# Optimization experiments

Hardware: AMD Instinct MI355X
Metric: run time of the kernel (lower is better)

## Reference

```python
import jax, jax.numpy as jnp
import numpy as np

HEADS = 16
EPS = 1e-5

def _ln(t):
    # LayerNorm over last axis, no affine params
    mu = jnp.mean(t, axis=-1, keepdims=True)
    var = jnp.var(t, axis=-1, keepdims=True)
    return (t - mu) / jnp.sqrt(var + EPS)

def setup_inputs() -> dict:
    key = jax.random.key(0)
    ks = jax.random.split(key, 8)
    b, n, dim, mlp_dim = 4, 2048, 1024, 4096
    s = lambda d: 1.0 / np.sqrt(d)
    return {
        "x": jax.random.normal(ks[0], (b, n, dim), dtype=jnp.float32),
        "Wqkv": jax.random.uniform(ks[1], (dim, 3 * dim), jnp.float32, -s(dim), s(dim)),
        "W1": jax.random.uniform(ks[2], (dim, mlp_dim), jnp.float32, -s(dim), s(dim)),
        "b1": jax.random.uniform(ks[3], (mlp_dim,), jnp.float32, -s(dim), s(dim)),
        "W2": jax.random.uniform(ks[4], (mlp_dim, dim), jnp.float32, -s(mlp_dim), s(mlp_dim)),
        "b2": jax.random.uniform(ks[5], (dim,), jnp.float32, -s(mlp_dim), s(mlp_dim)),
        "Wout": jax.random.uniform(ks[6], (dim, dim), jnp.float32, -s(dim), s(dim)),
        "bout": jax.random.uniform(ks[7], (dim,), jnp.float32, -s(dim), s(dim)),
    }

def reference(x, Wqkv, W1, b1, W2, b2, Wout, bout):
    b, n, dim = x.shape
    h = HEADS
    d = dim // h
    scale = dim ** (-0.5)  # NOTE: module scales by full dim, not head_dim
    qkv = x @ Wqkv  # [b, n, 3*dim]
    qkv = qkv.reshape(b, n, 3, h, d).transpose(2, 0, 3, 1, 4)  # [3, b, h, n, d]
    q, k, v = qkv[0], qkv[1], qkv[2]
    q, k = _ln(q), _ln(k)
    dots = jnp.einsum('bhid,bhjd->bhij', q, k) * scale
    attn = jax.nn.softmax(dots, axis=-1)
    attn_v = jnp.einsum('bhij,bhjd->bhid', attn, v)
    attn_v = attn_v.transpose(0, 2, 1, 3).reshape(b, n, dim)
    attn_out = attn_v @ Wout + bout
    parallel = jax.nn.gelu(x @ W1 + b1, approximate=False) @ W2 + b2
    return _ln(attn_out + parallel)
```

## Files before the change

kernel.cpp:

```cpp
#include <hip/hip_runtime.h>

typedef __attribute__((ext_vector_type(8))) short s16x8;
typedef __attribute__((ext_vector_type(4))) short s16x4;
typedef __attribute__((ext_vector_type(4))) float f32x4;
typedef __attribute__((ext_vector_type(16))) float f32x16;
typedef __attribute__((ext_vector_type(2))) unsigned uint2v;

#define DEVINL __device__ __forceinline__

DEVINL float b2f(short u){ return __uint_as_float(((unsigned)(unsigned short)u) << 16); }
DEVINL short f2bf(float f){
  unsigned u = __float_as_uint(f);
  u += 0x7fffu + ((u >> 16) & 1u);
  return (short)(u >> 16);
}
DEVINL unsigned cvtpk(float lo, float hi){
  unsigned r;
  asm("v_cvt_pk_bf16_f32 %0, %1, %2" : "=v"(r) : "v"(lo), "v"(hi));
  return r;
}
DEVINL float max3f(float a, float b, float c){
  float r; asm("v_max3_f32 %0, %1, %2, %3" : "=v"(r) : "v"(a), "v"(b), "v"(c)); return r;
}

#if __has_builtin(__builtin_amdgcn_exp2f)
#define EXP2F __builtin_amdgcn_exp2f
#else
#define EXP2F exp2f
#endif

DEVINL f32x4 mfma32(s16x8 a, s16x8 b, f32x4 c){
  return __builtin_amdgcn_mfma_f32_16x16x32_bf16(a, b, c, 0, 0, 0);
}
DEVINL f32x16 mfma3216(s16x8 a, s16x8 b, f32x16 c){
  return __builtin_amdgcn_mfma_f32_32x32x16_bf16(a, b, c, 0, 0, 0);
}

DEVINL uint2v pl32swap(unsigned a, unsigned b){
#if __has_builtin(__builtin_amdgcn_permlane32_swap)
  return __builtin_amdgcn_permlane32_swap(a, b, false, false);
#else
  asm volatile("v_permlane32_swap_b32 %0, %1" : "+v"(a), "+v"(b));
  uint2v r; r[0] = a; r[1] = b; return r;
#endif
}

typedef const unsigned __attribute__((address_space(1)))* gas1;
typedef unsigned __attribute__((address_space(3)))* las3;
DEVINL void gload16(const short* g, short* l){
  __builtin_amdgcn_global_load_lds((gas1)g, (las3)l, 16, 0, 0);
}

#define CFENCE asm volatile("" ::: "memory")
#define PBAR  do{ CFENCE; __builtin_amdgcn_sched_barrier(0); __builtin_amdgcn_s_barrier(); \
                  __builtin_amdgcn_sched_barrier(0); CFENCE; }while(0)
#define VMW8 asm volatile("s_waitcnt vmcnt(8)" ::: "memory")
#define VMW4 asm volatile("s_waitcnt vmcnt(4)" ::: "memory")
#define VMW0 asm volatile("s_waitcnt vmcnt(0)" ::: "memory")
#define PRIO1 __builtin_amdgcn_s_setprio(1)
#define PRIO0 __builtin_amdgcn_s_setprio(0)

static const int Bc   = 4;
static const int Nc   = 2048;
static const int DIM  = 1024;
static const int Tc   = Bc * Nc;
static const int MLP  = 4096;
static const int D3   = 3072;

static const size_t OFF_XB    = 0;
static const size_t OFF_WQKVT = OFF_XB    + 16777216;
static const size_t OFF_W1T   = OFF_WQKVT + 6291456;
static const size_t OFF_W2T   = OFF_W1T   + 8388608;
static const size_t OFF_WOUTT = OFF_W2T   + 8388608;
static const size_t OFF_QKV   = OFF_WOUTT + 2097152;
static const size_t OFF_QLN   = OFF_QKV   + 50331648;
static const size_t OFF_KLN   = OFF_QLN   + 16777216;
static const size_t OFF_VT    = OFF_KLN   + 16777216;
static const size_t OFF_ATTNV = OFF_VT    + 16777216;
static const size_t OFF_H     = OFF_QKV;
static const size_t OFF_P2    = OFF_KLN;
static const size_t OFF_A2    = OFF_VT;

__global__ __launch_bounds__(256) void conv_x(const float* __restrict__ x, short* __restrict__ xb){
  size_t i = ((size_t)blockIdx.x * 256 + threadIdx.x) * 8;
  f32x4 v0 = *(const f32x4*)(x + i);
  f32x4 v1 = *(const f32x4*)(x + i + 4);
  s16x8 o;
#pragma unroll
  for (int j = 0; j < 4; ++j){ o[j] = f2bf(v0[j]); o[4+j] = f2bf(v1[j]); }
  *(s16x8*)(xb + i) = o;
}

__global__ __launch_bounds__(256) void transpose_conv(const float* __restrict__ W, short* __restrict__ Wt,
                                                      int K, int N){
  __shared__ float tile[32][33];
  int ntx = N >> 5;
  int tx = blockIdx.x % ntx, ty = blockIdx.x / ntx;
  int r = threadIdx.x >> 3, c = (threadIdx.x & 7) * 4;
  f32x4 v = *(const f32x4*)(W + (size_t)(ty*32 + r)*N + tx*32 + c);
  tile[r][c] = v[0]; tile[r][c+1] = v[1]; tile[r][c+2] = v[2]; tile[r][c+3] = v[3];
  __syncthreads();
  s16x4 o;
#pragma unroll
  for (int j = 0; j < 4; ++j) o[j] = f2bf(tile[c+j][r]);
  *(s16x4*)(Wt + (size_t)(tx*32 + r)*K + ty*32 + c) = o;
}

template<int ACT>
__global__ __launch_bounds__(256, 2) void gemmCF(const short* __restrict__ A, const short* __restrict__ Bt,
                                                 short* __restrict__ C, const float* __restrict__ bias,
                                                 int M, int N, int K){
  __shared__ short lds[32768];

  const int tid = threadIdx.x;
  const int w = tid >> 6, lane = tid & 63;
  const int lr = lane & 15, g = lane >> 4;
  const int wr = w >> 1, wc = w & 1;
  const int NT = K >> 6, NIT = NT >> 1;

  const int nbn = N >> 7;
  const int cpx = gridDim.x >> 3;
  const int bid = (int)blockIdx.x;
  const int sw = (bid & 7)*cpx + (bid >> 3);
  const int nbn8 = nbn >> 3;
  const int T8 = sw >> 6, t64 = sw & 63;
  const int bm = (T8 / nbn8)*8 + (t64 >> 3);
  const int bn = (T8 % nbn8)*8 + (t64 & 7);

  const int l2 = lane >> 2;
  const int gsw = ((lane & 3) - ((lane >> 3) & 3)) & 3;
  const int cof = gsw * 8;
  const int qsw8 = ((g + (lr >> 1)) & 3) * 8;

  const short* ap0 = A  + (size_t)(bm*128 + w*16 + l2)*K + cof;
  const short* bp0 = Bt + (size_t)(bn*128 + w*16 + l2)*K + cof;

#define STG(soff, src, T_, kk) do{ \
    gload16(src + (size_t)(T_)*64 + (kk)*32,                 lds + (soff) + w*512); \
    gload16(src + (size_t)64*K + (size_t)(T_)*64 + (kk)*32,  lds + (soff) + 2048 + w*512); }while(0)
#define STA(s, T_, kk) STG((s)*4096, ap0, T_, kk)
#define STB(s, T_, kk) STG(16384 + (s)*4096, bp0, T_, kk)
#define LDA(s, mi) (*(const s16x8*)&lds[(s)*4096 + (wr*64 + (mi)*16 + lr)*32 + qsw8])
#define LDB(s, ni) (*(const s16x8*)&lds[16384 + (s)*4096 + (wc*64 + (ni)*16 + lr)*32 + qsw8])

  f32x4 acc[4][4] = {};
#define MM(ai, r) \
  acc[r][0]=mfma32(ai,b0,acc[r][0]); acc[r][1]=mfma32(ai,b1,acc[r][1]); \
  acc[r][2]=mfma32(ai,b2,acc[r][2]); acc[r][3]=mfma32(ai,b3,acc[r][3]);
#define RD(s) s16x8 a0=LDA(s,0),a1=LDA(s,1),a2=LDA(s,2),a3=LDA(s,3), \
                    b0=LDB(s,0),b1=LDB(s,1),b2=LDB(s,2),b3=LDB(s,3);
#define MM16 MM(a0,0) MM(a1,1) MM(a2,2) MM(a3,3)

  STA(0,0,0); STB(0,0,0);
  STA(1,0,1); STB(1,0,1);
  STA(2,1,0); STB(2,1,0);
  VMW8;
  PBAR;

  for (int i = 0; i < NIT; ++i){
    const int t = i << 1;
    const bool more = (i + 1 < NIT);
    {
      RD(0)
      STA(3, t+1, 1); STB(3, t+1, 1);
      PBAR; PRIO1; MM16 PRIO0;
      VMW8;
      PBAR;
    }
    {
      RD(1)
      if (more){ STA(0, t+2, 0); STB(0, t+2, 0); }
      PBAR; PRIO1; MM16 PRIO0;
      if (more){ VMW8; } else { VMW4; }
      PBAR;
    }
    {
      RD(2)
      if (more){ STA(1, t+2, 1); STB(1, t+2, 1); }
      PBAR; PRIO1; MM16 PRIO0;
      if (more){ VMW8; } else { VMW0; }
      PBAR;
    }
    {
      RD(3)
      if (more){ STA(2, t+3, 0); STB(2, t+3, 0); }
      PBAR; PRIO1; MM16 PRIO0;
      if (more){ VMW8; }
      PBAR;
    }
  }
#undef MM
#undef RD
#undef MM16
#undef STG
#undef STA
#undef STB
#undef LDA
#undef LDB

#pragma unroll
  for (int a = 0; a < 4; ++a){
#pragma unroll
    for (int ni = 0; ni < 4; ++ni){
      const int col = wc*64 + ni*16 + lr;
      const float bv = bias ? bias[bn*128 + col] : 0.f;
      f32x4 v = acc[a][ni];
#pragma unroll
      for (int ii = 0; ii < 4; ++ii){
        float val = v[ii] + bv;
        if constexpr (ACT) val = 0.5f*val*(1.f + erff(val*0.70710678118f));
        lds[(wr*64 + a*16 + 4*g + ii)*128 + col] = f2bf(val);
      }
    }
  }
  __syncthreads();
  const size_t crow0 = (size_t)bm * 128;
  const int ch = (tid & 15) * 8;
#pragma unroll
  for (int p = 0; p < 8; ++p){
    const int row = p*16 + (tid >> 4);
    *(s16x8*)&C[(crow0 + row)*N + bn*128 + ch] = *(const s16x8*)&lds[row*128 + ch];
  }
}

__global__ __launch_bounds__(256) void ln_reorg(const short* __restrict__ qkv, short* __restrict__ qln,
                                                short* __restrict__ kln, short* __restrict__ vtb){
  __shared__ short vtile[64*72];
  int bh = blockIdx.x >> 5, tch = blockIdx.x & 31;
  int b = bh >> 4, h = bh & 15;
  int tq = threadIdx.x >> 2, j = threadIdx.x & 3;
  size_t row = (size_t)b*Nc + tch*64 + tq;
  const short* base = qkv + row*D3 + h*64 + j*16;
  size_t orow = ((size_t)bh*Nc + tch*64 + tq)*64 + j*16;

#pragma unroll
  for (int part = 0; part < 2; ++part){
    const short* src = base + part*DIM;
    s16x8 u0 = *(const s16x8*)src;
    s16x8 u1 = *(const s16x8*)(src + 8);
    float f[16]; float s = 0.f, sq = 0.f;
#pragma unroll
    for (int i = 0; i < 8; ++i){ f[i] = b2f(u0[i]); f[8+i] = b2f(u1[i]); }
#pragma unroll
    for (int i = 0; i < 16; ++i){ s += f[i]; sq += f[i]*f[i]; }
    s  += __shfl_xor(s, 1);  s  += __shfl_xor(s, 2);
    sq += __shfl_xor(sq, 1); sq += __shfl_xor(sq, 2);
    float mu = s * (1.f/64.f);
    float var = sq * (1.f/64.f) - mu*mu;
    float inv = rsqrtf(var + 1e-5f) * (part == 0 ? 0.04508422003f : 1.f);
    s16x8 o0, o1;
#pragma unroll
    for (int i = 0; i < 8; ++i){ o0[i] = f2bf((f[i]-mu)*inv); o1[i] = f2bf((f[8+i]-mu)*inv); }
    short* dst = (part == 0 ? qln : kln) + orow;
    *(s16x8*)dst = o0; *(s16x8*)(dst + 8) = o1;
  }

  s16x8 v0 = *(const s16x8*)(base + 2*DIM);
  s16x8 v1 = *(const s16x8*)(base + 2*DIM + 8);
  *(s16x8*)&vtile[tq*72 + j*16]     = v0;
  *(s16x8*)&vtile[tq*72 + j*16 + 8] = v1;
  __syncthreads();
  s16x8 o0, o1;
#pragma unroll
  for (int i = 0; i < 8; ++i){
    o0[i] = vtile[(j*16 + i)*72 + tq];
    o1[i] = vtile[(j*16 + 8 + i)*72 + tq];
  }
  short* vdst = vtb + ((size_t)bh*64 + tq)*Nc + tch*64 + j*16;
  *(s16x8*)vdst = o0; *(s16x8*)(vdst + 8) = o1;
}

__global__ __launch_bounds__(256) void attn_kern(const short* __restrict__ qln, const short* __restrict__ kln,
                                                 const short* __restrict__ vtb, short* __restrict__ attnv){
  __shared__ short Ks[128*72];
  __shared__ short Vs[64*136];
  const int tid = threadIdx.x;
  const int bh = blockIdx.x >> 4, qt = blockIdx.x & 15;
  const int b = bh >> 4, h = bh & 15;
  const int w = tid >> 6, lane = tid & 63;
  const int lq = lane & 31, hi = lane >> 5;
  const int qrow = qt*128 + w*32 + lq;

  const short* qp = qln + ((size_t)bh*Nc + qrow)*64 + hi*8;
  s16x8 qf[4];
#pragma unroll
  for (int m = 0; m < 4; ++m) qf[m] = *(const s16x8*)(qp + m*16);

  f32x16 o0 = {0,0,0,0,0,0,0,0,0,0,0,0,0,0,0,0};
  f32x16 o1 = {0,0,0,0,0,0,0,0,0,0,0,0,0,0,0,0};
  float mrun = -INFINITY, l = 0.f;

  const short* kb0 = kln + (size_t)bh*Nc*64;
  const short* vb0 = vtb + (size_t)bh*64*Nc;
  const int vrow = tid >> 2, vq = tid & 3;

  s16x8 kr[4], vr[4];
#pragma unroll
  for (int j = 0; j < 4; ++j){
    kr[j] = *(const s16x8*)(kb0 + (size_t)(tid + j*256)*8);
    vr[j] = *(const s16x8*)(vb0 + (size_t)vrow*Nc + (vq + 4*j)*8);
  }

  for (int kt = 0; kt < 16; ++kt){
#pragma unroll
    for (int j = 0; j < 4; ++j){
      int s = tid + j*256;
      *(s16x8*)&Ks[(s>>3)*72 + (s&7)*8] = kr[j];
      *(s16x8*)&Vs[vrow*136 + (vq + 4*j)*8] = vr[j];
    }
    __syncthreads();
    if (kt + 1 < 16){
      const short* kb = kb0 + (size_t)(kt+1)*128*64;
      const short* vb = vb0 + (kt+1)*128;
#pragma unroll
      for (int j = 0; j < 4; ++j){
        kr[j] = *(const s16x8*)(kb + (size_t)(tid + j*256)*8);
        vr[j] = *(const s16x8*)(vb + (size_t)vrow*Nc + (vq + 4*j)*8);
      }
    }

#pragma unroll
    for (int kc = 0; kc < 4; ++kc){
      f32x16 st = {0,0,0,0,0,0,0,0,0,0,0,0,0,0,0,0};
#pragma unroll
      for (int m = 0; m < 4; ++m){
        s16x8 kf = *(const s16x8*)&Ks[(kc*32 + lq)*72 + m*16 + hi*8];
        st = mfma3216(kf, qf[m], st);
      }
      float cmax = max3f(st[0], st[1], st[2]);
      cmax = max3f(cmax, st[3], st[4]);
      cmax = max3f(cmax, st[5], st[6]);
      cmax = max3f(cmax, st[7], st[8]);
      cmax = max3f(cmax, st[9], st[10]);
      cmax = max3f(cmax, st[11], st[12]);
      cmax = max3f(cmax, st[13], st[14]);
      cmax = fmaxf(cmax, st[15]);
      cmax = fmaxf(cmax, __shfl_xor(cmax, 32));
      if (__any(cmax > mrun + 8.f)){
        float mnew = fmaxf(mrun, cmax);
        float fr = EXP2F(mrun - mnew);
        l *= fr;
#pragma unroll
        for (int r = 0; r < 16; ++r){ o0[r] *= fr; o1[r] *= fr; }
        mrun = mnew;
      }
      float p[16];
#pragma unroll
      for (int r = 0; r < 16; ++r){ p[r] = EXP2F(st[r] - mrun); l += p[r]; }

#pragma unroll
      for (int kh = 0; kh < 2; ++kh){
        int r0 = kh*8;
        unsigned wa = cvtpk(p[r0+0], p[r0+1]);
        unsigned wb = cvtpk(p[r0+4], p[r0+5]);
        unsigned wc2 = cvtpk(p[r0+2], p[r0+3]);
        unsigned wd = cvtpk(p[r0+6], p[r0+7]);
        uint2v s1 = pl32swap(wa, wb);
        uint2v s2 = pl32swap(wc2, wd);
        union { unsigned u[4]; s16x8 v; } pu;
        pu.u[0] = s1[0]; pu.u[1] = s2[0]; pu.u[2] = s1[1]; pu.u[3] = s2[1];
        s16x8 vf0 = *(const s16x8*)&Vs[ lq      *136 + kc*32 + kh*16 + hi*8];
        s16x8 vf1 = *(const s16x8*)&Vs[(32 + lq)*136 + kc*32 + kh*16 + hi*8];
        o0 = mfma3216(vf0, pu.v, o0);
        o1 = mfma3216(vf1, pu.v, o1);
      }
    }
    __syncthreads();
  }

  l += __shfl_xor(l, 32);
  float inv = 1.f / l;
  short* orow = attnv + ((size_t)(b*Nc + qrow))*DIM + h*64;
#pragma unroll
  for (int r = 0; r < 16; r += 2){
    int dv = (r&3) + 8*(r>>2) + 4*hi;
    *(unsigned*)&orow[dv]      = cvtpk(o0[r]*inv, o0[r+1]*inv);
    *(unsigned*)&orow[32 + dv] = cvtpk(o1[r]*inv, o1[r+1]*inv);
  }
}

__global__ __launch_bounds__(256) void final_ln(const short* __restrict__ a2, const short* __restrict__ p2,
                                                float* __restrict__ out){
  __shared__ float red[16];
  int row = blockIdx.x, tid = threadIdx.x;
  size_t base = (size_t)row*DIM + tid*4;
  s16x4 a = *(const s16x4*)(a2 + base);
  s16x4 p = *(const s16x4*)(p2 + base);
  float v[4]; float s = 0.f, sq = 0.f;
#pragma unroll
  for (int i = 0; i < 4; ++i){ v[i] = b2f(a[i]) + b2f(p[i]); s += v[i]; sq += v[i]*v[i]; }
#pragma unroll
  for (int m = 1; m < 64; m <<= 1){ s += __shfl_xor(s, m); sq += __shfl_xor(sq, m); }
  int wv = tid >> 6;
  if ((tid & 63) == 0){ red[wv] = s; red[8 + wv] = sq; }
  __syncthreads();
  if (tid == 0){
    float S = red[0] + red[1] + red[2] + red[3];
    float Q = red[8] + red[9] + red[10] + red[11];
    float mu = S * (1.f/1024.f);
    float var = Q * (1.f/1024.f) - mu*mu;
    red[12] = mu; red[13] = rsqrtf(var + 1e-5f);
  }
  __syncthreads();
  float mu = red[12], inv = red[13];
#pragma unroll
  for (int i = 0; i < 4; ++i) out[base + i] = (v[i] - mu) * inv;
}

extern "C" void kernel_launch(void* const* d_in, const int* in_sizes, int n_in,
                              void* d_out, int out_size, void* d_ws, size_t ws_size,
                              hipStream_t stream){
  const float* x    = (const float*)d_in[0];
  const float* Wqkv = (const float*)d_in[1];
  const float* W1   = (const float*)d_in[2];
  const float* b1   = (const float*)d_in[3];
  const float* W2   = (const float*)d_in[4];
  const float* b2   = (const float*)d_in[5];
  const float* Wout = (const float*)d_in[6];
  const float* bout = (const float*)d_in[7];
  float* out = (float*)d_out;
  char* ws = (char*)d_ws;

  short* xb    = (short*)(ws + OFF_XB);
  short* wqkvt = (short*)(ws + OFF_WQKVT);
  short* w1t   = (short*)(ws + OFF_W1T);
  short* w2t   = (short*)(ws + OFF_W2T);
  short* woutt = (short*)(ws + OFF_WOUTT);
  short* qkv   = (short*)(ws + OFF_QKV);
  short* qln   = (short*)(ws + OFF_QLN);
  short* kln   = (short*)(ws + OFF_KLN);
  short* vtb   = (short*)(ws + OFF_VT);
  short* attnv = (short*)(ws + OFF_ATTNV);
  short* hbuf  = (short*)(ws + OFF_H);
  short* p2    = (short*)(ws + OFF_P2);
  short* a2    = (short*)(ws + OFF_A2);

  conv_x<<<4096, 256, 0, stream>>>(x, xb);
  transpose_conv<<<(DIM/32)*(D3/32),  256, 0, stream>>>(Wqkv, wqkvt, DIM, D3);
  transpose_conv<<<(DIM/32)*(MLP/32), 256, 0, stream>>>(W1, w1t, DIM, MLP);
  transpose_conv<<<(MLP/32)*(DIM/32), 256, 0, stream>>>(W2, w2t, MLP, DIM);
  transpose_conv<<<(DIM/32)*(DIM/32), 256, 0, stream>>>(Wout, woutt, DIM, DIM);

  gemmCF<0><<<(Tc/128)*(D3/128),  256, 0, stream>>>(xb, wqkvt, qkv, nullptr, Tc, D3, DIM);
  ln_reorg<<<64*32, 256, 0, stream>>>(qkv, qln, kln, vtb);
  attn_kern<<<64*16, 256, 0, stream>>>(qln, kln, vtb, attnv);

  gemmCF<1><<<(Tc/128)*(MLP/128), 256, 0, stream>>>(xb, w1t, hbuf, b1, Tc, MLP, DIM);
  gemmCF<0><<<(Tc/128)*(DIM/128), 256, 0, stream>>>(hbuf, w2t, p2, b2, Tc, DIM, MLP);
  gemmCF<0><<<(Tc/128)*(DIM/128), 256, 0, stream>>>(attnv, woutt, a2, bout, Tc, DIM, DIM);

  final_ln<<<Tc, 256, 0, stream>>>(a2, p2, out);
}
```

Baseline: 421.9 us.

## Fuse W2 and Wout GEMMs via K-concatenation; double-buffer attention K/V tiles

The W2 and Wout projections become one GEMM over a concatenated K dimension (hbuf·W2 + attnv·Wout), with both biases added in the epilogue. The final LayerNorm then reads a single summed buffer, which removes one GEMM launch, one intermediate write and one read. The attention kernel switches to 64-key tiles held in double-buffered LDS, dropping the trailing barrier per tile in exchange for twice as many iterations. The K-concat path adds a branch on every staging load.

```diff
diff --git a/kernel.cpp b/kernel.cpp
--- a/kernel.cpp
+++ b/kernel.cpp
@@ -78,8 +78,7 @@
 static const size_t OFF_VT    = OFF_KLN   + 16777216;
 static const size_t OFF_ATTNV = OFF_VT    + 16777216;
 static const size_t OFF_H     = OFF_QKV;
-static const size_t OFF_P2    = OFF_KLN;
-static const size_t OFF_A2    = OFF_VT;
+static const size_t OFF_S2    = OFF_KLN;
 
 __global__ __launch_bounds__(256) void conv_x(const float* __restrict__ x, short* __restrict__ xb){
   size_t i = ((size_t)blockIdx.x * 256 + threadIdx.x) * 8;
@@ -106,17 +105,21 @@
   *(s16x4*)(Wt + (size_t)(tx*32 + r)*K + ty*32 + c) = o;
 }
 
-template<int ACT>
-__global__ __launch_bounds__(256, 2) void gemmCF(const short* __restrict__ A, const short* __restrict__ Bt,
-                                                 short* __restrict__ C, const float* __restrict__ bias,
-                                                 int M, int N, int K){
+template<int ACT, int FUSED>
+__global__ __launch_bounds__(256, 2) void gemmCF(const short* __restrict__ A, const short* __restrict__ A2,
+                                                 const short* __restrict__ Bt, const short* __restrict__ Bt2,
+                                                 short* __restrict__ C,
+                                                 const float* __restrict__ bias, const float* __restrict__ bias2,
+                                                 int M, int N, int K1, int K2){
   __shared__ short lds[32768];
 
   const int tid = threadIdx.x;
   const int w = tid >> 6, lane = tid & 63;
   const int lr = lane & 15, g = lane >> 4;
   const int wr = w >> 1, wc = w & 1;
-  const int NT = K >> 6, NIT = NT >> 1;
+  const int NT1 = K1 >> 6;
+  const int NT = NT1 + (FUSED ? (K2 >> 6) : 0);
+  const int NIT = NT >> 1;
 
   const int nbn = N >> 7;
   const int cpx = gridDim.x >> 3;
@@ -132,14 +135,36 @@
   const int cof = gsw * 8;
   const int qsw8 = ((g + (lr >> 1)) & 3) * 8;
 
-  const short* ap0 = A  + (size_t)(bm*128 + w*16 + l2)*K + cof;
-  const short* bp0 = Bt + (size_t)(bn*128 + w*16 + l2)*K + cof;
-
-#define STG(soff, src, T_, kk) do{ \
-    gload16(src + (size_t)(T_)*64 + (kk)*32,                 lds + (soff) + w*512); \
-    gload16(src + (size_t)64*K + (size_t)(T_)*64 + (kk)*32,  lds + (soff) + 2048 + w*512); }while(0)
-#define STA(s, T_, kk) STG((s)*4096, ap0, T_, kk)
-#define STB(s, T_, kk) STG(16384 + (s)*4096, bp0, T_, kk)
+  const short* ap0h = A  + (size_t)(bm*128 + w*16 + l2)*K1 + cof;
+  const short* bp0h = Bt + (size_t)(bn*128 + w*16 + l2)*K1 + cof;
+  const short* ap0a = FUSED ? (A2  + (size_t)(bm*128 + w*16 + l2)*K2 + cof) : nullptr;
+  const short* bp0a = FUSED ? (Bt2 + (size_t)(bn*128 + w*16 + l2)*K2 + cof) : nullptr;
+
+  auto stA = [&](int s, int T_, int kk){
+    short* d0 = lds + s*4096 + w*512;
+    if (FUSED && T_ >= NT1){
+      size_t off = (size_t)(T_ - NT1)*64 + kk*32;
+      gload16(ap0a + off, d0);
+      gload16(ap0a + (size_t)64*K2 + off, d0 + 2048);
+    } else {
+      size_t off = (size_t)T_*64 + kk*32;
+      gload16(ap0h + off, d0);
+      gload16(ap0h + (size_t)64*K1 + off, d0 + 2048);
+    }
+  };
+  auto stB = [&](int s, int T_, int kk){
+    short* d0 = lds + 16384 + s*4096 + w*512;
+    if (FUSED && T_ >= NT1){
+      size_t off = (size_t)(T_ - NT1)*64 + kk*32;
+      gload16(bp0a + off, d0);
+      gload16(bp0a + (size_t)64*K2 + off, d0 + 2048);
+    } else {
+      size_t off = (size_t)T_*64 + kk*32;
+      gload16(bp0h + off, d0);
+      gload16(bp0h + (size_t)64*K1 + off, d0 + 2048);
+    }
+  };
+
 #define LDA(s, mi) (*(const s16x8*)&lds[(s)*4096 + (wr*64 + (mi)*16 + lr)*32 + qsw8])
 #define LDB(s, ni) (*(const s16x8*)&lds[16384 + (s)*4096 + (wc*64 + (ni)*16 + lr)*32 + qsw8])
 
@@ -151,9 +176,9 @@
                     b0=LDB(s,0),b1=LDB(s,1),b2=LDB(s,2),b3=LDB(s,3);
 #define MM16 MM(a0,0) MM(a1,1) MM(a2,2) MM(a3,3)
 
-  STA(0,0,0); STB(0,0,0);
-  STA(1,0,1); STB(1,0,1);
-  STA(2,1,0); STB(2,1,0);
+  stA(0,0,0); stB(0,0,0);
+  stA(1,0,1); stB(1,0,1);
+  stA(2,1,0); stB(2,1,0);
   VMW8;
   PBAR;
 
@@ -162,28 +187,28 @@
     const bool more = (i + 1 < NIT);
     {
       RD(0)
-      STA(3, t+1, 1); STB(3, t+1, 1);
+      stA(3, t+1, 1); stB(3, t+1, 1);
       PBAR; PRIO1; MM16 PRIO0;
       VMW8;
       PBAR;
     }
     {
       RD(1)
-      if (more){ STA(0, t+2, 0); STB(0, t+2, 0); }
+      if (more){ stA(0, t+2, 0); stB(0, t+2, 0); }
       PBAR; PRIO1; MM16 PRIO0;
       if (more){ VMW8; } else { VMW4; }
       PBAR;
     }
     {
       RD(2)
-      if (more){ STA(1, t+2, 1); STB(1, t+2, 1); }
+      if (more){ stA(1, t+2, 1); stB(1, t+2, 1); }
       PBAR; PRIO1; MM16 PRIO0;
       if (more){ VMW8; } else { VMW0; }
       PBAR;
     }
     {
       RD(3)
-      if (more){ STA(2, t+3, 0); STB(2, t+3, 0); }
+      if (more){ stA(2, t+3, 0); stB(2, t+3, 0); }
       PBAR; PRIO1; MM16 PRIO0;
       if (more){ VMW8; }
       PBAR;
@@ -192,9 +217,6 @@
 #undef MM
 #undef RD
 #undef MM16
-#undef STG
-#undef STA
-#undef STB
 #undef LDA
 #undef LDB
 
@@ -203,7 +225,8 @@
 #pragma unroll
     for (int ni = 0; ni < 4; ++ni){
       const int col = wc*64 + ni*16 + lr;
-      const float bv = bias ? bias[bn*128 + col] : 0.f;
+      float bv = bias ? bias[bn*128 + col] : 0.f;
+      if (FUSED && bias2) bv += bias2[bn*128 + col];
       f32x4 v = acc[a][ni];
 #pragma unroll
       for (int ii = 0; ii < 4; ++ii){
@@ -272,8 +295,8 @@
 
 __global__ __launch_bounds__(256) void attn_kern(const short* __restrict__ qln, const short* __restrict__ kln,
                                                  const short* __restrict__ vtb, short* __restrict__ attnv){
-  __shared__ short Ks[128*72];
-  __shared__ short Vs[64*136];
+  __shared__ short Ks[2][64*72];
+  __shared__ short Vs[2][64*72];
   const int tid = threadIdx.x;
   const int bh = blockIdx.x >> 4, qt = blockIdx.x & 15;
   const int b = bh >> 4, h = bh & 15;
@@ -290,64 +313,73 @@
   f32x16 o1 = {0,0,0,0,0,0,0,0,0,0,0,0,0,0,0,0};
   float mrun = -INFINITY, l = 0.f;
 
+  const int sr = tid >> 3;
+  const int sc = (tid & 7) * 8;
   const short* kb0 = kln + (size_t)bh*Nc*64;
   const short* vb0 = vtb + (size_t)bh*64*Nc;
-  const int vrow = tid >> 2, vq = tid & 3;
-
-  s16x8 kr[4], vr[4];
-#pragma unroll
-  for (int j = 0; j < 4; ++j){
-    kr[j] = *(const s16x8*)(kb0 + (size_t)(tid + j*256)*8);
-    vr[j] = *(const s16x8*)(vb0 + (size_t)vrow*Nc + (vq + 4*j)*8);
-  }
-
-  for (int kt = 0; kt < 16; ++kt){
-#pragma unroll
-    for (int j = 0; j < 4; ++j){
-      int s = tid + j*256;
-      *(s16x8*)&Ks[(s>>3)*72 + (s&7)*8] = kr[j];
-      *(s16x8*)&Vs[vrow*136 + (vq + 4*j)*8] = vr[j];
-    }
+
+  s16x8 kr0, kr1, vr0, vr1;
+  {
+    kr0 = *(const s16x8*)(kb0 + (size_t)sr*64 + sc);
+    kr1 = *(const s16x8*)(kb0 + (size_t)(32 + sr)*64 + sc);
+    vr0 = *(const s16x8*)(vb0 + (size_t)sr*Nc + sc);
+    vr1 = *(const s16x8*)(vb0 + (size_t)(32 + sr)*Nc + sc);
+  }
+
+  for (int kt = 0; kt < 32; ++kt){
+    const int cur = kt & 1;
+    *(s16x8*)&Ks[cur][sr*72 + sc]        = kr0;
+    *(s16x8*)&Ks[cur][(32 + sr)*72 + sc] = kr1;
+    *(s16x8*)&Vs[cur][sr*72 + sc]        = vr0;
+    *(s16x8*)&Vs[cur][(32 + sr)*72 + sc] = vr1;
     __syncthreads();
-    if (kt + 1 < 16){
-      const short* kb = kb0 + (size_t)(kt+1)*128*64;
-      const short* vb = vb0 + (kt+1)*128;
-#pragma unroll
-      for (int j = 0; j < 4; ++j){
-        kr[j] = *(const s16x8*)(kb + (size_t)(tid + j*256)*8);
-        vr[j] = *(const s16x8*)(vb + (size_t)vrow*Nc + (vq + 4*j)*8);
-      }
-    }
-
-#pragma unroll
-    for (int kc = 0; kc < 4; ++kc){
-      f32x16 st = {0,0,0,0,0,0,0,0,0,0,0,0,0,0,0,0};
-#pragma unroll
-      for (int m = 0; m < 4; ++m){
-        s16x8 kf = *(const s16x8*)&Ks[(kc*32 + lq)*72 + m*16 + hi*8];
-        st = mfma3216(kf, qf[m], st);
-      }
-      float cmax = max3f(st[0], st[1], st[2]);
-      cmax = max3f(cmax, st[3], st[4]);
-      cmax = max3f(cmax, st[5], st[6]);
-      cmax = max3f(cmax, st[7], st[8]);
-      cmax = max3f(cmax, st[9], st[10]);
-      cmax = max3f(cmax, st[11], st[12]);
-      cmax = max3f(cmax, st[13], st[14]);
-      cmax = fmaxf(cmax, st[15]);
-      cmax = fmaxf(cmax, __shfl_xor(cmax, 32));
-      if (__any(cmax > mrun + 8.f)){
-        float mnew = fmaxf(mrun, cmax);
-        float fr = EXP2F(mrun - mnew);
-        l *= fr;
-#pragma unroll
-        for (int r = 0; r < 16; ++r){ o0[r] *= fr; o1[r] *= fr; }
-        mrun = mnew;
-      }
-      float p[16];
-#pragma unroll
-      for (int r = 0; r < 16; ++r){ p[r] = EXP2F(st[r] - mrun); l += p[r]; }
-
+    if (kt + 1 < 32){
+      const short* kb = kb0 + (size_t)(kt+1)*64*64;
+      const short* vb = vb0 + (kt+1)*64;
+      kr0 = *(const s16x8*)(kb + (size_t)sr*64 + sc);
+      kr1 = *(const s16x8*)(kb + (size_t)(32 + sr)*64 + sc);
+      vr0 = *(const s16x8*)(vb + (size_t)sr*Nc + sc);
+      vr1 = *(const s16x8*)(vb + (size_t)(32 + sr)*Nc + sc);
+    }
+
+    f32x16 st0 = {0,0,0,0,0,0,0,0,0,0,0,0,0,0,0,0};
+    f32x16 st1 = {0,0,0,0,0,0,0,0,0,0,0,0,0,0,0,0};
+#pragma unroll
+    for (int m = 0; m < 4; ++m){
+      s16x8 kf0 = *(const s16x8*)&Ks[cur][ lq      *72 + m*16 + hi*8];
+      s16x8 kf1 = *(const s16x8*)&Ks[cur][(32 + lq)*72 + m*16 + hi*8];
+      st0 = mfma3216(kf0, qf[m], st0);
+      st1 = mfma3216(kf1, qf[m], st1);
+    }
+
+    float cmax = max3f(st0[0], st0[1], st0[2]);
+    cmax = max3f(cmax, st0[3], st0[4]);   cmax = max3f(cmax, st0[5], st0[6]);
+    cmax = max3f(cmax, st0[7], st0[8]);   cmax = max3f(cmax, st0[9], st0[10]);
+    cmax = max3f(cmax, st0[11], st0[12]); cmax = max3f(cmax, st0[13], st0[14]);
+    cmax = max3f(cmax, st0[15], st1[0]);  cmax = max3f(cmax, st1[1], st1[2]);
+    cmax = max3f(cmax, st1[3], st1[4]);   cmax = max3f(cmax, st1[5], st1[6]);
+    cmax = max3f(cmax, st1[7], st1[8]);   cmax = max3f(cmax, st1[9], st1[10]);
+    cmax = max3f(cmax, st1[11], st1[12]); cmax = max3f(cmax, st1[13], st1[14]);
+    cmax = fmaxf(cmax, st1[15]);
+    cmax = fmaxf(cmax, __shfl_xor(cmax, 32));
+    if (__any(cmax > mrun + 8.f)){
+      float mnew = fmaxf(mrun, cmax);
+      float fr = EXP2F(mrun - mnew);
+      l *= fr;
+#pragma unroll
+      for (int r = 0; r < 16; ++r){ o0[r] *= fr; o1[r] *= fr; }
+      mrun = mnew;
+    }
+    float p0[16], p1[16];
+#pragma unroll
+    for (int r = 0; r < 16; ++r){
+      p0[r] = EXP2F(st0[r] - mrun); l += p0[r];
+      p1[r] = EXP2F(st1[r] - mrun); l += p1[r];
+    }
+
+#pragma unroll
+    for (int kc = 0; kc < 2; ++kc){
+      const float* p = kc ? p1 : p0;
 #pragma unroll
       for (int kh = 0; kh < 2; ++kh){
         int r0 = kh*8;
@@ -359,13 +391,12 @@
         uint2v s2 = pl32swap(wc2, wd);
         union { unsigned u[4]; s16x8 v; } pu;
         pu.u[0] = s1[0]; pu.u[1] = s2[0]; pu.u[2] = s1[1]; pu.u[3] = s2[1];
-        s16x8 vf0 = *(const s16x8*)&Vs[ lq      *136 + kc*32 + kh*16 + hi*8];
-        s16x8 vf1 = *(const s16x8*)&Vs[(32 + lq)*136 + kc*32 + kh*16 + hi*8];
+        s16x8 vf0 = *(const s16x8*)&Vs[cur][ lq      *72 + kc*32 + kh*16 + hi*8];
+        s16x8 vf1 = *(const s16x8*)&Vs[cur][(32 + lq)*72 + kc*32 + kh*16 + hi*8];
         o0 = mfma3216(vf0, pu.v, o0);
         o1 = mfma3216(vf1, pu.v, o1);
       }
     }
-    __syncthreads();
   }
 
   l += __shfl_xor(l, 32);
@@ -379,16 +410,14 @@
   }
 }
 
-__global__ __launch_bounds__(256) void final_ln(const short* __restrict__ a2, const short* __restrict__ p2,
-                                                float* __restrict__ out){
+__global__ __launch_bounds__(256) void final_ln(const short* __restrict__ s2, float* __restrict__ out){
   __shared__ float red[16];
   int row = blockIdx.x, tid = threadIdx.x;
   size_t base = (size_t)row*DIM + tid*4;
-  s16x4 a = *(const s16x4*)(a2 + base);
-  s16x4 p = *(const s16x4*)(p2 + base);
+  s16x4 a = *(const s16x4*)(s2 + base);
   float v[4]; float s = 0.f, sq = 0.f;
 #pragma unroll
-  for (int i = 0; i < 4; ++i){ v[i] = b2f(a[i]) + b2f(p[i]); s += v[i]; sq += v[i]*v[i]; }
+  for (int i = 0; i < 4; ++i){ v[i] = b2f(a[i]); s += v[i]; sq += v[i]*v[i]; }
 #pragma unroll
   for (int m = 1; m < 64; m <<= 1){ s += __shfl_xor(s, m); sq += __shfl_xor(sq, m); }
   int wv = tid >> 6;
@@ -432,8 +461,7 @@
   short* vtb   = (short*)(ws + OFF_VT);
   short* attnv = (short*)(ws + OFF_ATTNV);
   short* hbuf  = (short*)(ws + OFF_H);
-  short* p2    = (short*)(ws + OFF_P2);
-  short* a2    = (short*)(ws + OFF_A2);
+  short* s2    = (short*)(ws + OFF_S2);
 
   conv_x<<<4096, 256, 0, stream>>>(x, xb);
   transpose_conv<<<(DIM/32)*(D3/32),  256, 0, stream>>>(Wqkv, wqkvt, DIM, D3);
@@ -441,13 +469,15 @@
   transpose_conv<<<(MLP/32)*(DIM/32), 256, 0, stream>>>(W2, w2t, MLP, DIM);
   transpose_conv<<<(DIM/32)*(DIM/32), 256, 0, stream>>>(Wout, woutt, DIM, DIM);
 
-  gemmCF<0><<<(Tc/128)*(D3/128),  256, 0, stream>>>(xb, wqkvt, qkv, nullptr, Tc, D3, DIM);
+  gemmCF<0,0><<<(Tc/128)*(D3/128), 256, 0, stream>>>(xb, xb, wqkvt, wqkvt, qkv,
+                                                     nullptr, nullptr, Tc, D3, DIM, DIM);
   ln_reorg<<<64*32, 256, 0, stream>>>(qkv, qln, kln, vtb);
   attn_kern<<<64*16, 256, 0, stream>>>(qln, kln, vtb, attnv);
 
-  gemmCF<1><<<(Tc/128)*(MLP/128), 256, 0, stream>>>(xb, w1t, hbuf, b1, Tc, MLP, DIM);
-  gemmCF<0><<<(Tc/128)*(DIM/128), 256, 0, stream>>>(hbuf, w2t, p2, b2, Tc, DIM, MLP);
-  gemmCF<0><<<(Tc/128)*(DIM/128), 256, 0, stream>>>(attnv, woutt, a2, bout, Tc, DIM, DIM);
-
-  final_ln<<<Tc, 256, 0, stream>>>(a2, p2, out);
-}
+  gemmCF<1,0><<<(Tc/128)*(MLP/128), 256, 0, stream>>>(xb, xb, w1t, w1t, hbuf,
+                                                      b1, nullptr, Tc, MLP, DIM, DIM);
+  gemmCF<0,1><<<(Tc/128)*(DIM/128), 256, 0, stream>>>(hbuf, attnv, w2t, woutt, s2,
+                                                      b2, bout, Tc, DIM, MLP, DIM);
+
+  final_ln<<<Tc, 256, 0, stream>>>(s2, out);
+}
```

New measurement: 419.2 us. No clear change (-0.6%).
